# Performance work log

Measured on AMD Instinct MI355X. Metric: run time of the kernel, lower is better.

Reference implementation:

```python
import jax, jax.numpy as jnp
import numpy as np

B, T, IN_DIM, H = 32, 512, 2048, 512


def _lstm_layer(x, W_ih, W_hh, b_ih, b_hh):
    """Single LSTM layer, PyTorch gate order (i, f, g, o).
    x: [B, T, D] -> [B, T, H]
    """
    # Precompute input contribution for all timesteps in one GEMM.
    xg = jnp.einsum('btd,gd->btg', x, W_ih) + (b_ih + b_hh)  # [B, T, 4H]
    xg = jnp.transpose(xg, (1, 0, 2))  # [T, B, 4H] for scan over time
    h0 = jnp.zeros((x.shape[0], W_hh.shape[1]), x.dtype)
    c0 = jnp.zeros_like(h0)

    def step(carry, xg_t):
        h, c = carry
        gates = xg_t + h @ W_hh.T  # [B, 4H]
        i, f, g, o = jnp.split(gates, 4, axis=-1)
        i = jax.nn.sigmoid(i)
        f = jax.nn.sigmoid(f)
        g = jnp.tanh(g)
        o = jax.nn.sigmoid(o)
        c = f * c + i * g
        h = o * jnp.tanh(c)
        return (h, c), h

    _, hs = jax.lax.scan(step, (h0, c0), xg)  # hs: [T, B, H]
    return jnp.transpose(hs, (1, 0, 2))  # [B, T, H]


def setup_inputs() -> dict:
    key = jax.random.key(0)
    ks = jax.random.split(key, 9)
    k = 1.0 / np.sqrt(H)  # torch nn.LSTM init: U(-1/sqrt(H), 1/sqrt(H))

    def u(kk, shape):
        return jax.random.uniform(kk, shape, jnp.float32, -k, k)

    return {
        'feats_input': jax.random.normal(ks[0], (B, T, IN_DIM), jnp.float32),
        'W_ih0': u(ks[1], (4 * H, IN_DIM)),
        'W_hh0': u(ks[2], (4 * H, H)),
        'b_ih0': u(ks[3], (4 * H,)),
        'b_hh0': u(ks[4], (4 * H,)),
        'W_ih1': u(ks[5], (4 * H, H)),
        'W_hh1': u(ks[6], (4 * H, H)),
        'b_ih1': u(ks[7], (4 * H,)),
        'b_hh1': u(ks[8], (4 * H,)),
    }


def reference(feats_input, W_ih0, W_hh0, b_ih0, b_hh0, W_ih1, W_hh1, b_ih1, b_hh1):
    # 2-layer stacked LSTM, batch_first. Inter-layer dropout is identity
    # (inference / eval mode reference).
    h1 = _lstm_layer(feats_input, W_ih0, W_hh0, b_ih0, b_hh0)
    h2 = _lstm_layer(h1, W_ih1, W_hh1, b_ih1, b_hh1)
    return h2
```

## Files before the change

### kernel.cpp

```cpp
#include <hip/hip_runtime.h>

typedef __bf16 bf16x8 __attribute__((ext_vector_type(8)));
typedef float f32x4 __attribute__((ext_vector_type(4)));

static constexpr int B = 32, T = 512, IN = 2048, H = 512;
static constexpr int G4 = 4 * H;
static constexpr int M_ALL = B * T;
static constexpr int NWG = 16;
static constexpr unsigned NHALF = 8;

__device__ __forceinline__ ushort f2b(float f) {
  unsigned u = __float_as_uint(f);
  u = (u + 0x7FFFu + ((u >> 16) & 1u)) >> 16;
  return (ushort)u;
}
__device__ __forceinline__ float b2f(ushort h) {
  return __uint_as_float(((unsigned)h) << 16);
}
__device__ __forceinline__ float fast_sigmoid(float x) {
  float e = __expf(-x);
  return 1.0f / (1.0f + e);
}
__device__ __forceinline__ float fast_tanh(float x) {
  float ax = fabsf(x);
  float e = __expf(-2.0f * ax);
  float t = (1.0f - e) / (1.0f + e);
  return copysignf(t, x);
}
__device__ __forceinline__ void split8(const float4 a, const float4 b, uint4& hi, uint4& lo) {
  float x[8] = {a.x, a.y, a.z, a.w, b.x, b.y, b.z, b.w};
  ushort h[8], l[8];
#pragma unroll
  for (int i = 0; i < 8; ++i) {
    h[i] = f2b(x[i]);
    l[i] = f2b(x[i] - b2f(h[i]));
  }
  hi = make_uint4(h[0] | ((unsigned)h[1] << 16), h[2] | ((unsigned)h[3] << 16),
                  h[4] | ((unsigned)h[5] << 16), h[6] | ((unsigned)h[7] << 16));
  lo = make_uint4(l[0] | ((unsigned)l[1] << 16), l[2] | ((unsigned)l[3] << 16),
                  l[4] | ((unsigned)l[5] << 16), l[6] | ((unsigned)l[7] << 16));
}
__device__ __forceinline__ bf16x8 f2b8(const float* p) {
  float4 a = *(const float4*)p, b = *(const float4*)(p + 4);
  uint4 u;
  u.x = f2b(a.x) | ((unsigned)f2b(a.y) << 16);
  u.y = f2b(a.z) | ((unsigned)f2b(a.w) << 16);
  u.z = f2b(b.x) | ((unsigned)f2b(b.y) << 16);
  u.w = f2b(b.z) | ((unsigned)f2b(b.w) << 16);
  return __builtin_bit_cast(bf16x8, u);
}

__device__ __forceinline__ void st_coh_u16(void* p, ushort v) {
  unsigned vv = v;
  asm volatile("global_store_short %0, %1, off sc1" :: "v"(p), "v"(vv) : "memory");
}
__device__ __forceinline__ void wait_vm0() {
  asm volatile("s_waitcnt vmcnt(0)" ::: "memory");
}

template <int AMODE>
__global__ __launch_bounds__(256) void gemm3(
    const float* __restrict__ Af, const ushort* __restrict__ Abf,
    const float* __restrict__ Bf,
    const float* __restrict__ bias1, const float* __restrict__ bias2,
    float* __restrict__ C, int M, int N, int K) {
  __shared__ ushort AsH[128][40], AsL[128][40], BsH[128][40], BsL[128][40];
  const int m0 = blockIdx.x * 128, n0 = blockIdx.y * 128;
  const int tid = threadIdx.x, lane = tid & 63, wave = tid >> 6;
  const int wm = (wave & 1) * 64, wn = (wave >> 1) * 64;
  const int lrow = lane & 15, lq = lane >> 4;
  const int sr = tid >> 2;
  const int sk = (tid & 3) * 8;

  f32x4 acc[4][4] = {};

  for (int k0 = 0; k0 < K; k0 += 32) {
    __syncthreads();
#pragma unroll
    for (int half = 0; half < 2; ++half) {
      const int r = sr + half * 64;
      if constexpr (AMODE == 0) {
        const float* p = Af + (long)(m0 + r) * K + k0 + sk;
        uint4 hi, lo;
        split8(*(const float4*)p, *(const float4*)(p + 4), hi, lo);
        *(uint4*)&AsH[r][sk] = hi;
        *(uint4*)&AsL[r][sk] = lo;
      } else {
        *(uint4*)&AsH[r][sk] = *(const uint4*)(Abf + (long)(m0 + r) * K + k0 + sk);
      }
      const float* q = Bf + (long)(n0 + r) * K + k0 + sk;
      uint4 bh, bl;
      split8(*(const float4*)q, *(const float4*)(q + 4), bh, bl);
      *(uint4*)&BsH[r][sk] = bh;
      *(uint4*)&BsL[r][sk] = bl;
    }
    __syncthreads();
    bf16x8 aH[4], aL[4], bH[4], bL[4];
#pragma unroll
    for (int i = 0; i < 4; ++i) {
      aH[i] = __builtin_bit_cast(bf16x8, *(const uint4*)&AsH[wm + i * 16 + lrow][lq * 8]);
      if constexpr (AMODE == 0)
        aL[i] = __builtin_bit_cast(bf16x8, *(const uint4*)&AsL[wm + i * 16 + lrow][lq * 8]);
      bH[i] = __builtin_bit_cast(bf16x8, *(const uint4*)&BsH[wn + i * 16 + lrow][lq * 8]);
      bL[i] = __builtin_bit_cast(bf16x8, *(const uint4*)&BsL[wn + i * 16 + lrow][lq * 8]);
    }
#pragma unroll
    for (int mt = 0; mt < 4; ++mt)
#pragma unroll
      for (int nt = 0; nt < 4; ++nt) {
        acc[mt][nt] = __builtin_amdgcn_mfma_f32_16x16x32_bf16(aH[mt], bH[nt], acc[mt][nt], 0, 0, 0);
        acc[mt][nt] = __builtin_amdgcn_mfma_f32_16x16x32_bf16(aH[mt], bL[nt], acc[mt][nt], 0, 0, 0);
        if constexpr (AMODE == 0)
          acc[mt][nt] = __builtin_amdgcn_mfma_f32_16x16x32_bf16(aL[mt], bH[nt], acc[mt][nt], 0, 0, 0);
      }
  }

#pragma unroll
  for (int mt = 0; mt < 4; ++mt)
#pragma unroll
    for (int nt = 0; nt < 4; ++nt) {
      const int col = n0 + wn + nt * 16 + lrow;
      const float bsum = bias1[col] + bias2[col];
#pragma unroll
      for (int r = 0; r < 4; ++r) {
        const int row = m0 + wm + mt * 16 + lq * 4 + r;
        C[(long)row * N + col] = acc[mt][nt][r] + bsum;
      }
    }
}

__global__ __launch_bounds__(256, 1) void lstm_scan(
    const float* __restrict__ Whh,
    const float* __restrict__ xg,
    ushort* __restrict__ seq_bf,
    float* __restrict__ seq_f32,
    ushort* __restrict__ hbuf,
    unsigned* __restrict__ cnt) {
  const int tid = threadIdx.x, lane = tid & 63;
  const int half = blockIdx.x >> 3;
  const int j0 = ((blockIdx.x & 7) * 4 + (tid >> 6)) * 16;
  const int b0 = half * 16;
  const int lrow = lane & 15, lq = lane >> 4;
  unsigned* mycnt = cnt + half * T;

  bf16x8 Wf[4][16];
#pragma unroll
  for (int q = 0; q < 4; ++q)
#pragma unroll
    for (int kt = 0; kt < 16; ++kt)
      Wf[q][kt] = f2b8(Whh + (long)(q * 512 + j0 + lrow) * 512 + kt * 32 + lq * 8);

  float c[4] = {0.f, 0.f, 0.f, 0.f};
  const float* xgb = xg + (long)(b0 + lq * 4) * T * G4 + j0 + lrow;
  const ushort* hld = hbuf + (b0 + lrow) * H + lq * 8;

  for (int t = 0; t < T; ++t) {
    float xgv[4][4];
#pragma unroll
    for (int q = 0; q < 4; ++q)
#pragma unroll
      for (int r = 0; r < 4; ++r)
        xgv[q][r] = xgb[((long)r * T + t) * G4 + q * 512];

    f32x4 acc[4] = {};
    if (t > 0) {
      if (tid == 0)
        while (__hip_atomic_load(&mycnt[t - 1], __ATOMIC_RELAXED, __HIP_MEMORY_SCOPE_AGENT) < NHALF)
          __builtin_amdgcn_s_sleep(1);
      __syncthreads();
      const unsigned long long* hp64 =
          (const unsigned long long*)(hld + (size_t)(t & 1) * (B * H));
      unsigned long long hw[32];
#pragma unroll
      for (int kt = 0; kt < 16; ++kt) {
        hw[2 * kt] = __hip_atomic_load(hp64 + kt * 8, __ATOMIC_RELAXED, __HIP_MEMORY_SCOPE_AGENT);
        hw[2 * kt + 1] = __hip_atomic_load(hp64 + kt * 8 + 1, __ATOMIC_RELAXED, __HIP_MEMORY_SCOPE_AGENT);
      }
#pragma unroll
      for (int kt = 0; kt < 16; ++kt) {
        const uint4 hv = make_uint4(
            (unsigned)hw[2 * kt], (unsigned)(hw[2 * kt] >> 32),
            (unsigned)hw[2 * kt + 1], (unsigned)(hw[2 * kt + 1] >> 32));
        const bf16x8 ah = __builtin_bit_cast(bf16x8, hv);
#pragma unroll
        for (int q = 0; q < 4; ++q)
          acc[q] = __builtin_amdgcn_mfma_f32_16x16x32_bf16(ah, Wf[q][kt], acc[q], 0, 0, 0);
      }
    }

    ushort* hn = hbuf + (size_t)((t + 1) & 1) * (B * H);
#pragma unroll
    for (int r = 0; r < 4; ++r) {
      const float iv = fast_sigmoid(acc[0][r] + xgv[0][r]);
      const float fv = fast_sigmoid(acc[1][r] + xgv[1][r]);
      const float gv = fast_tanh(acc[2][r] + xgv[2][r]);
      const float ov = fast_sigmoid(acc[3][r] + xgv[3][r]);
      c[r] = fv * c[r] + iv * gv;
      const float h = ov * fast_tanh(c[r]);
      const int b = b0 + lq * 4 + r, j = j0 + lrow;
      const ushort hb = f2b(h);
      st_coh_u16(hn + b * H + j, hb);
      if (seq_bf) seq_bf[((long)b * T + t) * H + j] = hb;
      if (seq_f32) seq_f32[((long)b * T + t) * H + j] = h;
    }
    wait_vm0();
    __syncthreads();
    if (tid == 0)
      __hip_atomic_fetch_add(&mycnt[t], 1u, __ATOMIC_RELAXED, __HIP_MEMORY_SCOPE_AGENT);
  }
}

extern "C" void kernel_launch(void* const* d_in, const int* in_sizes, int n_in,
                              void* d_out, int out_size, void* d_ws, size_t ws_size,
                              hipStream_t stream) {
  const float* feats = (const float*)d_in[0];
  const float* Wih0 = (const float*)d_in[1];
  const float* Whh0 = (const float*)d_in[2];
  const float* bih0 = (const float*)d_in[3];
  const float* bhh0 = (const float*)d_in[4];
  const float* Wih1 = (const float*)d_in[5];
  const float* Whh1 = (const float*)d_in[6];
  const float* bih1 = (const float*)d_in[7];
  const float* bhh1 = (const float*)d_in[8];

  char* ws = (char*)d_ws;
  float* xg      = (float*)(ws + 0);
  ushort* seq    = (ushort*)(ws + 134217728);
  ushort* hbuf   = (ushort*)(ws + 150994944);
  unsigned* cnt  = (unsigned*)(ws + 151060480);

  hipMemsetAsync(cnt, 0, 4 * T * sizeof(unsigned), stream);

  gemm3<0><<<dim3(M_ALL / 128, G4 / 128), dim3(256), 0, stream>>>(
      feats, nullptr, Wih0, bih0, bhh0, xg, M_ALL, G4, IN);

  lstm_scan<<<dim3(NWG), dim3(256), 0, stream>>>(
      Whh0, xg, seq, nullptr, hbuf, cnt);

  gemm3<2><<<dim3(M_ALL / 128, G4 / 128), dim3(256), 0, stream>>>(
      nullptr, seq, Wih1, bih1, bhh1, xg, M_ALL, G4, H);

  lstm_scan<<<dim3(NWG), dim3(256), 0, stream>>>(
      Whh1, xg, nullptr, (float*)d_out, hbuf, cnt + 2 * T);
}
```

Measured before the change: 7.916 ms.

## Split LSTM recurrent matmul K dimension across two waves with LDS reduction

Doubles the scan workgroup to 512 threads and splits the 512-wide hidden-state K dimension between wave pairs. Each wave now holds half the recurrent weights and does half the MFMAs, and the partial sums are reduced through shared memory before the gate math. The goal is to shorten per-step latency on the serial critical path. The cost is an extra LDS round trip and barrier per timestep, with gate and output work falling on half the waves.

```diff
diff --git a/kernel.cpp b/kernel.cpp
--- a/kernel.cpp
+++ b/kernel.cpp
@@ -129,7 +129,7 @@
     }
 }
 
-__global__ __launch_bounds__(256, 1) void lstm_scan(
+__global__ __launch_bounds__(512, 2) void lstm_scan(
     const float* __restrict__ Whh,
     const float* __restrict__ xg,
     ushort* __restrict__ seq_bf,
@@ -137,18 +137,23 @@
     ushort* __restrict__ hbuf,
     unsigned* __restrict__ cnt) {
   const int tid = threadIdx.x, lane = tid & 63;
+  const int wave = tid >> 6;
+  const int jl = wave >> 1;
+  const int ksel = wave & 1;
   const int half = blockIdx.x >> 3;
-  const int j0 = ((blockIdx.x & 7) * 4 + (tid >> 6)) * 16;
+  const int j0 = ((blockIdx.x & 7) * 4 + jl) * 16;
   const int b0 = half * 16;
   const int lrow = lane & 15, lq = lane >> 4;
   unsigned* mycnt = cnt + half * T;
 
-  bf16x8 Wf[4][16];
+  bf16x8 Wf[4][8];
 #pragma unroll
   for (int q = 0; q < 4; ++q)
 #pragma unroll
-    for (int kt = 0; kt < 16; ++kt)
-      Wf[q][kt] = f2b8(Whh + (long)(q * 512 + j0 + lrow) * 512 + kt * 32 + lq * 8);
+    for (int k = 0; k < 8; ++k)
+      Wf[q][k] = f2b8(Whh + (long)(q * 512 + j0 + lrow) * 512 + (ksel * 8 + k) * 32 + lq * 8);
+
+  __shared__ float4 red[4][4][64];
 
   float c[4] = {0.f, 0.f, 0.f, 0.f};
   const float* xgb = xg + (long)(b0 + lq * 4) * T * G4 + j0 + lrow;
@@ -156,54 +161,73 @@
 
   for (int t = 0; t < T; ++t) {
     float xgv[4][4];
-#pragma unroll
-    for (int q = 0; q < 4; ++q)
-#pragma unroll
-      for (int r = 0; r < 4; ++r)
-        xgv[q][r] = xgb[((long)r * T + t) * G4 + q * 512];
-
-    f32x4 acc[4] = {};
+    if (ksel == 0) {
+#pragma unroll
+      for (int q = 0; q < 4; ++q)
+#pragma unroll
+        for (int r = 0; r < 4; ++r)
+          xgv[q][r] = xgb[((long)r * T + t) * G4 + q * 512];
+    }
+
     if (t > 0) {
       if (tid == 0)
         while (__hip_atomic_load(&mycnt[t - 1], __ATOMIC_RELAXED, __HIP_MEMORY_SCOPE_AGENT) < NHALF)
           __builtin_amdgcn_s_sleep(1);
       __syncthreads();
+    }
+
+    f32x4 acc[4] = {};
+    if (t > 0) {
       const unsigned long long* hp64 =
           (const unsigned long long*)(hld + (size_t)(t & 1) * (B * H));
-      unsigned long long hw[32];
-#pragma unroll
-      for (int kt = 0; kt < 16; ++kt) {
-        hw[2 * kt] = __hip_atomic_load(hp64 + kt * 8, __ATOMIC_RELAXED, __HIP_MEMORY_SCOPE_AGENT);
-        hw[2 * kt + 1] = __hip_atomic_load(hp64 + kt * 8 + 1, __ATOMIC_RELAXED, __HIP_MEMORY_SCOPE_AGENT);
-      }
-#pragma unroll
-      for (int kt = 0; kt < 16; ++kt) {
+      unsigned long long hw[16];
+#pragma unroll
+      for (int k = 0; k < 8; ++k) {
+        const int kt = ksel * 8 + k;
+        hw[2 * k] = __hip_atomic_load(hp64 + kt * 8, __ATOMIC_RELAXED, __HIP_MEMORY_SCOPE_AGENT);
+        hw[2 * k + 1] = __hip_atomic_load(hp64 + kt * 8 + 1, __ATOMIC_RELAXED, __HIP_MEMORY_SCOPE_AGENT);
+      }
+#pragma unroll
+      for (int k = 0; k < 8; ++k) {
         const uint4 hv = make_uint4(
-            (unsigned)hw[2 * kt], (unsigned)(hw[2 * kt] >> 32),
-            (unsigned)hw[2 * kt + 1], (unsigned)(hw[2 * kt + 1] >> 32));
+            (unsigned)hw[2 * k], (unsigned)(hw[2 * k] >> 32),
+            (unsigned)hw[2 * k + 1], (unsigned)(hw[2 * k + 1] >> 32));
         const bf16x8 ah = __builtin_bit_cast(bf16x8, hv);
 #pragma unroll
         for (int q = 0; q < 4; ++q)
-          acc[q] = __builtin_amdgcn_mfma_f32_16x16x32_bf16(ah, Wf[q][kt], acc[q], 0, 0, 0);
-      }
-    }
-
-    ushort* hn = hbuf + (size_t)((t + 1) & 1) * (B * H);
-#pragma unroll
-    for (int r = 0; r < 4; ++r) {
-      const float iv = fast_sigmoid(acc[0][r] + xgv[0][r]);
-      const float fv = fast_sigmoid(acc[1][r] + xgv[1][r]);
-      const float gv = fast_tanh(acc[2][r] + xgv[2][r]);
-      const float ov = fast_sigmoid(acc[3][r] + xgv[3][r]);
-      c[r] = fv * c[r] + iv * gv;
-      const float h = ov * fast_tanh(c[r]);
-      const int b = b0 + lq * 4 + r, j = j0 + lrow;
-      const ushort hb = f2b(h);
-      st_coh_u16(hn + b * H + j, hb);
-      if (seq_bf) seq_bf[((long)b * T + t) * H + j] = hb;
-      if (seq_f32) seq_f32[((long)b * T + t) * H + j] = h;
-    }
-    wait_vm0();
+          acc[q] = __builtin_amdgcn_mfma_f32_16x16x32_bf16(ah, Wf[q][k], acc[q], 0, 0, 0);
+      }
+    }
+
+    if (ksel == 1) {
+#pragma unroll
+      for (int i = 0; i < 4; ++i)
+        red[jl][i][lane] = __builtin_bit_cast(float4, acc[i]);
+    }
+    __syncthreads();
+    if (ksel == 0) {
+#pragma unroll
+      for (int i = 0; i < 4; ++i) {
+        const float4 p = red[jl][i][lane];
+        acc[i][0] += p.x; acc[i][1] += p.y; acc[i][2] += p.z; acc[i][3] += p.w;
+      }
+      ushort* hn = hbuf + (size_t)((t + 1) & 1) * (B * H);
+#pragma unroll
+      for (int r = 0; r < 4; ++r) {
+        const float iv = fast_sigmoid(acc[0][r] + xgv[0][r]);
+        const float fv = fast_sigmoid(acc[1][r] + xgv[1][r]);
+        const float gv = fast_tanh(acc[2][r] + xgv[2][r]);
+        const float ov = fast_sigmoid(acc[3][r] + xgv[3][r]);
+        c[r] = fv * c[r] + iv * gv;
+        const float h = ov * fast_tanh(c[r]);
+        const int b = b0 + lq * 4 + r, j = j0 + lrow;
+        const ushort hb = f2b(h);
+        st_coh_u16(hn + b * H + j, hb);
+        if (seq_bf) seq_bf[((long)b * T + t) * H + j] = hb;
+        if (seq_f32) seq_f32[((long)b * T + t) * H + j] = h;
+      }
+      wait_vm0();
+    }
     __syncthreads();
     if (tid == 0)
       __hip_atomic_fetch_add(&mycnt[t], 1u, __ATOMIC_RELAXED, __HIP_MEMORY_SCOPE_AGENT);
@@ -234,12 +258,12 @@
   gemm3<0><<<dim3(M_ALL / 128, G4 / 128), dim3(256), 0, stream>>>(
       feats, nullptr, Wih0, bih0, bhh0, xg, M_ALL, G4, IN);
 
-  lstm_scan<<<dim3(NWG), dim3(256), 0, stream>>>(
+  lstm_scan<<<dim3(NWG), dim3(512), 0, stream>>>(
       Whh0, xg, seq, nullptr, hbuf, cnt);
 
   gemm3<2><<<dim3(M_ALL / 128, G4 / 128), dim3(256), 0, stream>>>(
       nullptr, seq, Wih1, bih1, bhh1, xg, M_ALL, G4, H);
 
-  lstm_scan<<<dim3(NWG), dim3(256), 0, stream>>>(
+  lstm_scan<<<dim3(NWG), dim3(512), 0, stream>>>(
       Whh1, xg, nullptr, (float*)d_out, hbuf, cnt + 2 * T);
 }
```

Result: faster. 7.628 ms (-3.6%).
